# Kernel optimization log

Hardware: AMD Instinct MI355X
Metric: run time of the kernel (lower is better)

## Reference

```python
import jax, jax.numpy as jnp
import numpy as np

D = 2048        # input_size / model dim
H = 2816        # hidden_size per expert (GLU -> w1 has 2*H rows)
E = 8           # num_experts
M = 4096        # tokens (batch*seq)


def setup_inputs() -> dict:
    key = jax.random.key(0)
    k1, k2, k3, k4, k5 = jax.random.split(key, 5)
    x = jax.random.normal(k1, (M, D), dtype=jnp.float32)
    # ParallelExperts init: uniform(-1/fan_in_dim, 1/fan_in_dim); scale kept simple here
    w1 = jax.random.uniform(k2, (E, 2 * H, D), dtype=jnp.float32, minval=-1.0, maxval=1.0) / (2 * H)
    w2 = jax.random.uniform(k3, (E, D, H), dtype=jnp.float32, minval=-1.0, maxval=1.0) / D
    router_w = jax.random.normal(k4, (E, D), dtype=jnp.float32) * (1.0 / np.sqrt(D))
    bias = jnp.zeros((D,), dtype=jnp.float32)
    return {"x": x, "w1": w1, "w2": w2, "router_w": router_w, "bias": bias, "top_k": 2}


def _moe_forward(x, w1, w2, router_w, bias, top_k):
    # Router: logits -> softmax (fp32) -> top-k -> renormalize (fused_moe semantics)
    logits = x @ router_w.T                                # [M, E]
    probs = jax.nn.softmax(logits.astype(jnp.float32), axis=-1)
    topk_w, topk_ids = jax.lax.top_k(probs, top_k)         # [M, k]
    topk_w = topk_w / jnp.sum(topk_w, axis=-1, keepdims=True)
    # Dense combine weights [M, E]: gate weight if expert selected, else 0
    m = x.shape[0]
    combine = jnp.zeros((m, w1.shape[0]), dtype=x.dtype)
    combine = combine.at[jnp.arange(m)[:, None], topk_ids].add(topk_w.astype(x.dtype))
    # Grouped expert GEMMs, expressed as a loop over the small fixed expert set.
    # Contribution of expert e is masked by combine[:, e] (zero for unrouted tokens).
    y = jnp.zeros_like(x)
    hdim = w2.shape[2]
    for e in range(w1.shape[0]):
        g = x @ w1[e].T                                    # [M, 2H]
        h = jax.nn.silu(g[:, :hdim]) * g[:, hdim:]          # silu_and_mul (GLU)
        y = y + combine[:, e:e + 1] * (h @ w2[e].T)         # [M, D]
    return y + bias


def reference(x, w1, w2, router_w, bias, top_k):
    return _moe_forward(x, w1, w2, router_w, bias, top_k)
```

## Files before the change

kernel.cpp:

```cpp
#include <hip/hip_runtime.h>
#include <hip/hip_bf16.h>
#include <stdint.h>

#define M_TOK 4096
#define DDIM  2048
#define HDIM  2816
#define NEXP  8
#define PMAX  10240
#define MAXTILES 40
#define NB1   22
#define NB2   16
#define NKT1  32
#define NKT2  44

typedef __attribute__((ext_vector_type(8))) short short8;
typedef __attribute__((ext_vector_type(4))) float f32x4;

#define GLD16(g, l) __builtin_amdgcn_global_load_lds(                              \
    (const __attribute__((address_space(1))) unsigned int*)(g),                    \
    (__attribute__((address_space(3))) unsigned int*)(l), 16, 0, 0)

#define VMCNT(n) asm volatile("s_waitcnt vmcnt(" #n ")" ::: "memory")

__device__ __forceinline__ unsigned short f2bf(float f) {
  unsigned int u = __float_as_uint(f);
  u += 0x7fffu + ((u >> 16) & 1u);
  return (unsigned short)(u >> 16);
}
__device__ __forceinline__ float bf2f(unsigned short u) {
  return __uint_as_float(((unsigned)u) << 16);
}

#define STGA(TT, PP, S)                                                            \
  { size_t kb_ = (size_t)(TT) * 128 + (S) * 64;                                    \
    char* d_ = ldsp + (PP) * 32768 + (S) * 16384;                                  \
    GLD16(aS0 + kb_, d_ + tid * 16); GLD16(aS1 + kb_, d_ + 8192 + tid * 16); }

#define STGB(TT, PP, S)                                                            \
  { size_t kb_ = (size_t)(TT) * 128 + (S) * 64;                                    \
    char* d_ = ldsp + 65536 + (PP) * 32768 + (S) * 16384;                          \
    GLD16(bS0 + kb_, d_ + tid * 16); GLD16(bS1 + kb_, d_ + 8192 + tid * 16); }

#define DSRA(PP, S, M)                                                             \
  { const char* ab_ = ldsp + (PP) * 32768 + (S) * 16384;                           \
    _Pragma("unroll") for (int j_ = 0; j_ < 4; ++j_)                               \
      av[j_] = *(const short8*)(ab_ + aoff[(M) * 4 + j_]); }

#define DSRB(PP, S)                                                                \
  { const char* bb_ = ldsp + 65536 + (PP) * 32768 + (S) * 16384;                   \
    _Pragma("unroll") for (int j_ = 0; j_ < 4; ++j_)                               \
      bv[j_] = *(const short8*)(bb_ + boff[j_]); }

#define MMA16(M)                                                                   \
  { __builtin_amdgcn_s_setprio(1);                                                 \
    _Pragma("unroll") for (int j_ = 0; j_ < 4; ++j_)                               \
      _Pragma("unroll") for (int n_ = 0; n_ < 4; ++n_)                             \
        acc[(M) * 4 + j_][n_] =                                                    \
          __builtin_amdgcn_mfma_f32_16x16x32_bf16(av[j_], bv[n_], acc[(M)*4+j_][n_], 0, 0, 0); \
    __builtin_amdgcn_s_setprio(0); }

#define KTILE(T, P, S0, S1, S2, S3, VM)                                            \
  { DSRA(P, 0, 0); DSRB(P, 0);                                                     \
    if (S0) STGA((T) + 1, (P) ^ 1, 1);                                             \
    __builtin_amdgcn_s_barrier(); MMA16(0); __builtin_amdgcn_s_barrier();          \
    DSRA(P, 0, 1);                                                                 \
    if (S1) STGB((T) + 2, P, 0);                                                   \
    __builtin_amdgcn_s_barrier(); MMA16(1); __builtin_amdgcn_s_barrier();          \
    DSRA(P, 1, 0); DSRB(P, 1);                                                     \
    if (S2) STGA((T) + 2, P, 0);                                                   \
    __builtin_amdgcn_s_barrier(); MMA16(0); __builtin_amdgcn_s_barrier();          \
    DSRA(P, 1, 1);                                                                 \
    if (S3) STGB((T) + 2, P, 1);                                                   \
    __builtin_amdgcn_s_barrier(); MMA16(1);                                        \
    VMCNT(VM);                                                                     \
    __builtin_amdgcn_s_barrier(); }

__global__ void init_k(int* __restrict__ tok, int* __restrict__ counts, int* __restrict__ cursors) {
  int i = blockIdx.x * blockDim.x + threadIdx.x;
  if (i < PMAX) tok[i] = -1;
  if (i < NEXP) { counts[i] = 0; cursors[i] = 0; }
}

__global__ __launch_bounds__(256) void router_cvt_k(const float4* __restrict__ x4,
                                                    const float4* __restrict__ rw4,
                                                    ushort4* __restrict__ xb4,
                                                    float* __restrict__ wgt,
                                                    int* __restrict__ eid,
                                                    int* __restrict__ counts,
                                                    const float4* __restrict__ w14,
                                                    ushort4* __restrict__ w1b4,
                                                    const float4* __restrict__ w24,
                                                    ushort4* __restrict__ w2b4) {
  int lane = threadIdx.x & 63;
  int wv = threadIdx.x >> 6;
  int t = blockIdx.x * 4 + wv;
  int base = t * (DDIM / 4);
  float acc[NEXP];
#pragma unroll
  for (int e = 0; e < NEXP; ++e) acc[e] = 0.f;
#pragma unroll
  for (int j = 0; j < DDIM / 4 / 64; ++j) {
    float4 v = x4[base + j * 64 + lane];
    ushort4 o;
    o.x = f2bf(v.x); o.y = f2bf(v.y); o.z = f2bf(v.z); o.w = f2bf(v.w);
    xb4[base + j * 64 + lane] = o;
#pragma unroll
    for (int e = 0; e < NEXP; ++e) {
      float4 w = rw4[e * (DDIM / 4) + j * 64 + lane];
      acc[e] += v.x * w.x + v.y * w.y + v.z * w.z + v.w * w.w;
    }
  }
#pragma unroll
  for (int e = 0; e < NEXP; ++e) {
#pragma unroll
    for (int s = 32; s > 0; s >>= 1) acc[e] += __shfl_xor(acc[e], s, 64);
  }
  if (lane == 0) {
    float mx = acc[0];
#pragma unroll
    for (int e = 1; e < NEXP; ++e) mx = fmaxf(mx, acc[e]);
    float p[NEXP];
#pragma unroll
    for (int e = 0; e < NEXP; ++e) p[e] = expf(acc[e] - mx);
    int e0 = 0; float p0 = p[0];
#pragma unroll
    for (int e = 1; e < NEXP; ++e) if (p[e] > p0) { p0 = p[e]; e0 = e; }
    int e1 = -1; float p1 = -1.f;
#pragma unroll
    for (int e = 0; e < NEXP; ++e) if (e != e0 && p[e] > p1) { p1 = p[e]; e1 = e; }
    float s = p0 + p1;
    wgt[2 * t] = p0 / s; wgt[2 * t + 1] = p1 / s;
    eid[2 * t] = e0;     eid[2 * t + 1] = e1;
    atomicAdd(&counts[e0], 1);
    atomicAdd(&counts[e1], 1);
  }
  const int n1 = NEXP * 2 * HDIM * DDIM / 4;
  const int n2 = NEXP * DDIM * HDIM / 4;
  const int stride = (M_TOK / 4) * 256;
  int id = blockIdx.x * 256 + threadIdx.x;
  for (int i = id; i < n1; i += stride) {
    float4 v = w14[i];
    ushort4 o;
    o.x = f2bf(v.x); o.y = f2bf(v.y); o.z = f2bf(v.z); o.w = f2bf(v.w);
    w1b4[i] = o;
  }
  for (int i = id; i < n2; i += stride) {
    float4 v = w24[i];
    ushort4 o;
    o.x = f2bf(v.x); o.y = f2bf(v.y); o.z = f2bf(v.z); o.w = f2bf(v.w);
    w2b4[i] = o;
  }
}

__global__ void offsets_k(const int* __restrict__ counts, int* __restrict__ offs,
                          int* __restrict__ tile2exp, int* __restrict__ tilerow,
                          int* __restrict__ ntiles) {
  if (threadIdx.x == 0 && blockIdx.x == 0) {
    int o = 0, nt = 0;
    for (int e = 0; e < NEXP; ++e) {
      offs[e] = o;
      int c = counts[e];
      int pt = (c + 255) >> 8;
      for (int i = 0; i < pt; ++i) { tile2exp[nt] = e; tilerow[nt] = o + i * 256; ++nt; }
      o += pt << 8;
    }
    offs[NEXP] = o;
    ntiles[0] = nt;
  }
}

__global__ void scatter_k(const int* __restrict__ eid, const int* __restrict__ offs,
                          int* __restrict__ cursors, int* __restrict__ tok,
                          int* __restrict__ slot) {
  int t = blockIdx.x * blockDim.x + threadIdx.x;
  if (t >= M_TOK) return;
#pragma unroll
  for (int k = 0; k < 2; ++k) {
    int e = eid[2 * t + k];
    int p = offs[e] + atomicAdd(&cursors[e], 1);
    tok[p] = t;
    slot[2 * t + k] = p;
  }
}

__global__ __launch_bounds__(512, 1) void gemm1_k(const unsigned short* __restrict__ xb,
                                                  const unsigned short* __restrict__ w1b,
                                                  const int* __restrict__ tok,
                                                  const int* __restrict__ tile2exp,
                                                  const int* __restrict__ tilerow,
                                                  const int* __restrict__ ntiles,
                                                  unsigned short* __restrict__ h) {
  __shared__ char ldsp[131072];
  int mt = blockIdx.x;
  if (mt >= ntiles[0]) return;
  int e = tile2exp[mt], r0 = tilerow[mt];
  int n0 = blockIdx.y * 128;
  int tid = threadIdx.x, lane = tid & 63;
  int wv = tid >> 6, wm = wv >> 2, wn = wv & 3;
  int l15 = lane & 15, g = lane >> 4;

  int row0 = tid >> 2, g0 = (tid & 3) ^ ((row0 >> 1) & 3);
  int row1 = row0 + 128;
  int t0 = tok[r0 + row0]; if (t0 < 0) t0 = 0;
  int t1 = tok[r0 + row1]; if (t1 < 0) t1 = 0;
  const char* aS0 = (const char*)xb + (size_t)t0 * (DDIM * 2) + g0 * 16;
  const char* aS1 = (const char*)xb + (size_t)t1 * (DDIM * 2) + g0 * 16;
  size_t w1r0 = (size_t)e * (2 * HDIM) + (size_t)(n0 + row0);
  size_t w1r1 = (size_t)e * (2 * HDIM) + (size_t)(HDIM + n0 + row0);
  const char* bS0 = (const char*)w1b + w1r0 * (DDIM * 2) + g0 * 16;
  const char* bS1 = (const char*)w1b + w1r1 * (DDIM * 2) + g0 * 16;

  int aoff[8], boff[4];
#pragma unroll
  for (int mi = 0; mi < 8; ++mi) {
    int r = wm * 128 + mi * 16 + l15;
    aoff[mi] = r * 64 + ((g ^ ((r >> 1) & 3)) << 4);
  }
#pragma unroll
  for (int ni = 0; ni < 4; ++ni) {
    int r = wn * 64 + ni * 16 + l15;
    boff[ni] = r * 64 + ((g ^ ((r >> 1) & 3)) << 4);
  }

  f32x4 acc[8][4];
#pragma unroll
  for (int mi = 0; mi < 8; ++mi)
#pragma unroll
    for (int ni = 0; ni < 4; ++ni) acc[mi][ni] = (f32x4)(0.f);

  short8 av[4], bv[4];

  STGA(0, 0, 0); STGB(0, 0, 0); STGA(0, 0, 1); STGB(0, 0, 1);
  STGB(1, 1, 0); STGA(1, 1, 0); STGB(1, 1, 1);
  VMCNT(6);
  __builtin_amdgcn_s_barrier();

#pragma unroll 1
  for (int t = 0; t < NKT1 - 2; t += 2) {
    KTILE(t, 0, 1, 1, 1, 1, 6);
    KTILE(t + 1, 1, 1, 1, 1, 1, 6);
  }
  KTILE(NKT1 - 2, 0, 1, 0, 0, 0, 0);
  KTILE(NKT1 - 1, 1, 0, 0, 0, 0, 0);

  __syncthreads();
  float* xch = (float*)ldsp;
  int rbase = (lane >> 4) * 4;
  if (wn >= 2) {
    int uc0 = (wn - 2) * 64;
#pragma unroll
    for (int mi = 0; mi < 8; ++mi)
#pragma unroll
      for (int ni = 0; ni < 4; ++ni)
#pragma unroll
        for (int j = 0; j < 4; ++j) {
          int r = wm * 128 + mi * 16 + rbase + j;
          int c = uc0 + ni * 16 + l15;
          int cs = c ^ ((r & 3) << 2) ^ ((r & 1) << 4);
          xch[r * 128 + cs] = acc[mi][ni][j];
        }
  }
  __syncthreads();
  if (wn < 2) {
#pragma unroll
    for (int mi = 0; mi < 8; ++mi)
#pragma unroll
      for (int ni = 0; ni < 4; ++ni)
#pragma unroll
        for (int j = 0; j < 4; ++j) {
          int r = wm * 128 + mi * 16 + rbase + j;
          int c = wn * 64 + ni * 16 + l15;
          int cs = c ^ ((r & 3) << 2) ^ ((r & 1) << 4);
          float gg = acc[mi][ni][j];
          float u = xch[r * 128 + cs];
          float sv = gg / (1.f + expf(-gg));
          h[(size_t)(r0 + r) * HDIM + n0 + c] = f2bf(sv * u);
        }
  }
}

__global__ __launch_bounds__(256, 2) void gemm2_k(const unsigned short* __restrict__ h,
                                                  const unsigned short* __restrict__ w2b,
                                                  const int* __restrict__ tile2exp,
                                                  const int* __restrict__ tilerow,
                                                  const int* __restrict__ ntiles,
                                                  unsigned short* __restrict__ yp) {
  __shared__ char ldsp[49152];
  int mt = blockIdx.x;
  if (mt >= ntiles[0]) return;
  int e = tile2exp[mt], r0 = tilerow[mt];
  int n0 = blockIdx.y * 128;
  int tid = threadIdx.x, lane = tid & 63;
  int wv = tid >> 6, wm = wv >> 1, wn = wv & 1;
  int l15 = lane & 15, lq = lane >> 4;

  int sg = tid & 7, srow = tid >> 3;
  unsigned int aOff[8], bOff[4];
#pragma unroll
  for (int j = 0; j < 8; ++j) {
    int r = j * 32 + srow;
    aOff[j] = (unsigned int)(r0 + r) * (HDIM * 2) + (unsigned int)((sg ^ (r & 7)) << 4);
  }
#pragma unroll
  for (int j = 0; j < 4; ++j) {
    int r = j * 32 + srow;
    bOff[j] = (unsigned int)(e * DDIM + n0 + r) * (HDIM * 2) + (unsigned int)((sg ^ (r & 7)) << 4);
  }

  int aRd[8], bRd[4];
#pragma unroll
  for (int i = 0; i < 8; ++i) {
    int r = wm * 128 + i * 16 + l15;
    aRd[i] = r * 128 + ((lq ^ (r & 7)) << 4);
  }
#pragma unroll
  for (int i = 0; i < 4; ++i) {
    int r = wn * 64 + i * 16 + l15;
    bRd[i] = r * 128 + ((lq ^ (r & 7)) << 4);
  }

  f32x4 acc[8][4];
#pragma unroll
  for (int mi = 0; mi < 8; ++mi)
#pragma unroll
    for (int ni = 0; ni < 4; ++ni) acc[mi][ni] = (f32x4)(0.f);

  const char* hB = (const char*)h;
  const char* wB = (const char*)w2b;

#pragma unroll 1
  for (int kt = 0; kt < NKT2; ++kt) {
    __syncthreads();
    unsigned int kb = (unsigned int)kt * 128;
#pragma unroll
    for (int j = 0; j < 8; ++j) GLD16(hB + aOff[j] + kb, ldsp + j * 4096 + tid * 16);
#pragma unroll
    for (int j = 0; j < 4; ++j) GLD16(wB + bOff[j] + kb, ldsp + 32768 + j * 4096 + tid * 16);
    VMCNT(0);
    __syncthreads();
#pragma unroll
    for (int kh = 0; kh < 2; ++kh) {
      int kx = kh << 6;
      short8 a[8], b[4];
#pragma unroll
      for (int i = 0; i < 8; ++i) a[i] = *(const short8*)(ldsp + (aRd[i] ^ kx));
#pragma unroll
      for (int i = 0; i < 4; ++i) b[i] = *(const short8*)(ldsp + 32768 + (bRd[i] ^ kx));
      __builtin_amdgcn_s_setprio(1);
#pragma unroll
      for (int mi = 0; mi < 8; ++mi)
#pragma unroll
        for (int ni = 0; ni < 4; ++ni)
          acc[mi][ni] = __builtin_amdgcn_mfma_f32_16x16x32_bf16(a[mi], b[ni], acc[mi][ni], 0, 0, 0);
      __builtin_amdgcn_s_setprio(0);
    }
  }

#pragma unroll
  for (int mi = 0; mi < 8; ++mi)
#pragma unroll
    for (int ni = 0; ni < 4; ++ni)
#pragma unroll
      for (int j = 0; j < 4; ++j) {
        int r = r0 + wm * 128 + mi * 16 + lq * 4 + j;
        int c = n0 + wn * 64 + ni * 16 + l15;
        yp[(size_t)r * DDIM + c] = f2bf(acc[mi][ni][j]);
      }
}

__global__ void combine_k(const unsigned short* __restrict__ yp, const float* __restrict__ wgt,
                          const int* __restrict__ slot, const float* __restrict__ bias,
                          float* __restrict__ out) {
  int idx = blockIdx.x * blockDim.x + threadIdx.x;
  int t = idx >> 8, q = (idx & 255) * 8;
  float w0 = wgt[2 * t], w1 = wgt[2 * t + 1];
  int s0 = slot[2 * t], s1 = slot[2 * t + 1];
  short8 a8 = *(const short8*)(yp + (size_t)s0 * DDIM + q);
  short8 b8 = *(const short8*)(yp + (size_t)s1 * DDIM + q);
  float* op = out + (size_t)t * DDIM + q;
#pragma unroll
  for (int k = 0; k < 8; ++k) {
    float av = bf2f((unsigned short)a8[k]);
    float bv = bf2f((unsigned short)b8[k]);
    op[k] = w0 * av + w1 * bv + bias[q + k];
  }
}

extern "C" void kernel_launch(void* const* d_in, const int* in_sizes, int n_in,
                              void* d_out, int out_size, void* d_ws, size_t ws_size,
                              hipStream_t stream) {
  const float* x    = (const float*)d_in[0];
  const float* w1   = (const float*)d_in[1];
  const float* w2   = (const float*)d_in[2];
  const float* rw   = (const float*)d_in[3];
  const float* bias = (const float*)d_in[4];
  float* out = (float*)d_out;

  char* ws = (char*)d_ws;
  size_t off = 0;
  auto alloc = [&](size_t bytes) -> void* {
    void* p = ws + off;
    off = (off + bytes + 255) & ~(size_t)255;
    return p;
  };
  unsigned short* w1b = (unsigned short*)alloc((size_t)NEXP * 2 * HDIM * DDIM * 2);
  unsigned short* w2b = (unsigned short*)alloc((size_t)NEXP * DDIM * HDIM * 2);
  unsigned short* xb  = (unsigned short*)alloc((size_t)M_TOK * DDIM * 2);
  unsigned short* h   = (unsigned short*)alloc((size_t)PMAX * HDIM * 2);
  unsigned short* yp  = (unsigned short*)alloc((size_t)PMAX * DDIM * 2);
  float* wgt          = (float*)alloc((size_t)M_TOK * 2 * 4);
  int* eid            = (int*)alloc((size_t)M_TOK * 2 * 4);
  int* slot           = (int*)alloc((size_t)M_TOK * 2 * 4);
  int* tok            = (int*)alloc((size_t)PMAX * 4);
  int* counts         = (int*)alloc(64 * 4);
  int* cursors        = (int*)alloc(64 * 4);
  int* offs           = (int*)alloc(64 * 4);
  int* ntiles         = (int*)alloc(64 * 4);
  int* tile2exp       = (int*)alloc(128 * 4);
  int* tilerow        = (int*)alloc(128 * 4);

  hipLaunchKernelGGL(init_k, dim3((PMAX + 255) / 256), dim3(256), 0, stream, tok, counts, cursors);
  hipLaunchKernelGGL(router_cvt_k, dim3(M_TOK / 4), dim3(256), 0, stream,
                     (const float4*)x, (const float4*)rw, (ushort4*)xb, wgt, eid, counts,
                     (const float4*)w1, (ushort4*)w1b, (const float4*)w2, (ushort4*)w2b);
  hipLaunchKernelGGL(offsets_k, dim3(1), dim3(64), 0, stream, counts, offs,
                     tile2exp, tilerow, ntiles);
  hipLaunchKernelGGL(scatter_k, dim3((M_TOK + 255) / 256), dim3(256), 0, stream, eid, offs, cursors, tok, slot);
  hipLaunchKernelGGL(gemm1_k, dim3(MAXTILES, NB1), dim3(512), 0, stream,
                     xb, w1b, tok, tile2exp, tilerow, ntiles, h);
  hipLaunchKernelGGL(gemm2_k, dim3(MAXTILES, NB2), dim3(256), 0, stream,
                     h, w2b, tile2exp, tilerow, ntiles, yp);
  hipLaunchKernelGGL(combine_k, dim3(M_TOK * (DDIM / 8) / 256), dim3(256), 0, stream, yp, wgt, slot, bias, out);
}
```

Before: 757.5 us.

## Split weight conversion from router and simplify gemm1 to single-buffered 256-thread tiles

Moves the fp32-to-bf16 weight conversion out of the router kernel into a separate grid-stride kernel that processes two elements per thread. gemm1 is rewritten from a 512-thread, double-buffered, 256x256 tile pipeline to a 256-thread kernel with a 256x128 tile (64 gate and 64 up columns), a single LDS buffer, and two blocks per CU. Each K step loads, waits fully and synchronizes before the MFMAs, so load and compute no longer overlap within a block. The change counts on the extra resident block to hide memory latency instead.

```diff
diff --git a/kernel.cpp b/kernel.cpp
--- a/kernel.cpp
+++ b/kernel.cpp
@@ -8,7 +8,7 @@
 #define NEXP  8
 #define PMAX  10240
 #define MAXTILES 40
-#define NB1   22
+#define NB1   44
 #define NB2   16
 #define NKT1  32
 #define NKT2  44
@@ -31,49 +31,28 @@
   return __uint_as_float(((unsigned)u) << 16);
 }
 
-#define STGA(TT, PP, S)                                                            \
-  { size_t kb_ = (size_t)(TT) * 128 + (S) * 64;                                    \
-    char* d_ = ldsp + (PP) * 32768 + (S) * 16384;                                  \
-    GLD16(aS0 + kb_, d_ + tid * 16); GLD16(aS1 + kb_, d_ + 8192 + tid * 16); }
-
-#define STGB(TT, PP, S)                                                            \
-  { size_t kb_ = (size_t)(TT) * 128 + (S) * 64;                                    \
-    char* d_ = ldsp + 65536 + (PP) * 32768 + (S) * 16384;                          \
-    GLD16(bS0 + kb_, d_ + tid * 16); GLD16(bS1 + kb_, d_ + 8192 + tid * 16); }
-
-#define DSRA(PP, S, M)                                                             \
-  { const char* ab_ = ldsp + (PP) * 32768 + (S) * 16384;                           \
-    _Pragma("unroll") for (int j_ = 0; j_ < 4; ++j_)                               \
-      av[j_] = *(const short8*)(ab_ + aoff[(M) * 4 + j_]); }
-
-#define DSRB(PP, S)                                                                \
-  { const char* bb_ = ldsp + 65536 + (PP) * 32768 + (S) * 16384;                   \
-    _Pragma("unroll") for (int j_ = 0; j_ < 4; ++j_)                               \
-      bv[j_] = *(const short8*)(bb_ + boff[j_]); }
-
-#define MMA16(M)                                                                   \
-  { __builtin_amdgcn_s_setprio(1);                                                 \
-    _Pragma("unroll") for (int j_ = 0; j_ < 4; ++j_)                               \
-      _Pragma("unroll") for (int n_ = 0; n_ < 4; ++n_)                             \
-        acc[(M) * 4 + j_][n_] =                                                    \
-          __builtin_amdgcn_mfma_f32_16x16x32_bf16(av[j_], bv[n_], acc[(M)*4+j_][n_], 0, 0, 0); \
-    __builtin_amdgcn_s_setprio(0); }
-
-#define KTILE(T, P, S0, S1, S2, S3, VM)                                            \
-  { DSRA(P, 0, 0); DSRB(P, 0);                                                     \
-    if (S0) STGA((T) + 1, (P) ^ 1, 1);                                             \
-    __builtin_amdgcn_s_barrier(); MMA16(0); __builtin_amdgcn_s_barrier();          \
-    DSRA(P, 0, 1);                                                                 \
-    if (S1) STGB((T) + 2, P, 0);                                                   \
-    __builtin_amdgcn_s_barrier(); MMA16(1); __builtin_amdgcn_s_barrier();          \
-    DSRA(P, 1, 0); DSRB(P, 1);                                                     \
-    if (S2) STGA((T) + 2, P, 0);                                                   \
-    __builtin_amdgcn_s_barrier(); MMA16(0); __builtin_amdgcn_s_barrier();          \
-    DSRA(P, 1, 1);                                                                 \
-    if (S3) STGB((T) + 2, P, 1);                                                   \
-    __builtin_amdgcn_s_barrier(); MMA16(1);                                        \
-    VMCNT(VM);                                                                     \
-    __builtin_amdgcn_s_barrier(); }
+__global__ void cvt2_bf16_k(const float4* __restrict__ in1, ushort4* __restrict__ out1, int n1,
+                            const float4* __restrict__ in2, ushort4* __restrict__ out2, int n2) {
+  const int stride = gridDim.x * blockDim.x;
+  const int total = n1 + n2;
+  int i = blockIdx.x * blockDim.x + threadIdx.x;
+  for (; i + stride < total; i += 2 * stride) {
+    int ia = i, ib = i + stride;
+    float4 va = (ia < n1) ? in1[ia] : in2[ia - n1];
+    float4 vb = (ib < n1) ? in1[ib] : in2[ib - n1];
+    ushort4 oa, ob;
+    oa.x = f2bf(va.x); oa.y = f2bf(va.y); oa.z = f2bf(va.z); oa.w = f2bf(va.w);
+    ob.x = f2bf(vb.x); ob.y = f2bf(vb.y); ob.z = f2bf(vb.z); ob.w = f2bf(vb.w);
+    if (ia < n1) out1[ia] = oa; else out2[ia - n1] = oa;
+    if (ib < n1) out1[ib] = ob; else out2[ib - n1] = ob;
+  }
+  if (i < total) {
+    float4 v = (i < n1) ? in1[i] : in2[i - n1];
+    ushort4 o;
+    o.x = f2bf(v.x); o.y = f2bf(v.y); o.z = f2bf(v.z); o.w = f2bf(v.w);
+    if (i < n1) out1[i] = o; else out2[i - n1] = o;
+  }
+}
 
 __global__ void init_k(int* __restrict__ tok, int* __restrict__ counts, int* __restrict__ cursors) {
   int i = blockIdx.x * blockDim.x + threadIdx.x;
@@ -81,16 +60,12 @@
   if (i < NEXP) { counts[i] = 0; cursors[i] = 0; }
 }
 
-__global__ __launch_bounds__(256) void router_cvt_k(const float4* __restrict__ x4,
-                                                    const float4* __restrict__ rw4,
-                                                    ushort4* __restrict__ xb4,
-                                                    float* __restrict__ wgt,
-                                                    int* __restrict__ eid,
-                                                    int* __restrict__ counts,
-                                                    const float4* __restrict__ w14,
-                                                    ushort4* __restrict__ w1b4,
-                                                    const float4* __restrict__ w24,
-                                                    ushort4* __restrict__ w2b4) {
+__global__ __launch_bounds__(256) void router_k(const float4* __restrict__ x4,
+                                                const float4* __restrict__ rw4,
+                                                ushort4* __restrict__ xb4,
+                                                float* __restrict__ wgt,
+                                                int* __restrict__ eid,
+                                                int* __restrict__ counts) {
   int lane = threadIdx.x & 63;
   int wv = threadIdx.x >> 6;
   int t = blockIdx.x * 4 + wv;
@@ -133,22 +108,6 @@
     eid[2 * t] = e0;     eid[2 * t + 1] = e1;
     atomicAdd(&counts[e0], 1);
     atomicAdd(&counts[e1], 1);
-  }
-  const int n1 = NEXP * 2 * HDIM * DDIM / 4;
-  const int n2 = NEXP * DDIM * HDIM / 4;
-  const int stride = (M_TOK / 4) * 256;
-  int id = blockIdx.x * 256 + threadIdx.x;
-  for (int i = id; i < n1; i += stride) {
-    float4 v = w14[i];
-    ushort4 o;
-    o.x = f2bf(v.x); o.y = f2bf(v.y); o.z = f2bf(v.z); o.w = f2bf(v.w);
-    w1b4[i] = o;
-  }
-  for (int i = id; i < n2; i += stride) {
-    float4 v = w24[i];
-    ushort4 o;
-    o.x = f2bf(v.x); o.y = f2bf(v.y); o.z = f2bf(v.z); o.w = f2bf(v.w);
-    w2b4[i] = o;
   }
 }
 
@@ -183,43 +142,47 @@
   }
 }
 
-__global__ __launch_bounds__(512, 1) void gemm1_k(const unsigned short* __restrict__ xb,
+__global__ __launch_bounds__(256, 2) void gemm1_k(const unsigned short* __restrict__ xb,
                                                   const unsigned short* __restrict__ w1b,
                                                   const int* __restrict__ tok,
                                                   const int* __restrict__ tile2exp,
                                                   const int* __restrict__ tilerow,
                                                   const int* __restrict__ ntiles,
                                                   unsigned short* __restrict__ h) {
-  __shared__ char ldsp[131072];
+  __shared__ char ldsp[65536];
   int mt = blockIdx.x;
   if (mt >= ntiles[0]) return;
   int e = tile2exp[mt], r0 = tilerow[mt];
-  int n0 = blockIdx.y * 128;
+  int n0 = blockIdx.y * 64;
   int tid = threadIdx.x, lane = tid & 63;
-  int wv = tid >> 6, wm = wv >> 2, wn = wv & 3;
-  int l15 = lane & 15, g = lane >> 4;
-
-  int row0 = tid >> 2, g0 = (tid & 3) ^ ((row0 >> 1) & 3);
-  int row1 = row0 + 128;
-  int t0 = tok[r0 + row0]; if (t0 < 0) t0 = 0;
-  int t1 = tok[r0 + row1]; if (t1 < 0) t1 = 0;
-  const char* aS0 = (const char*)xb + (size_t)t0 * (DDIM * 2) + g0 * 16;
-  const char* aS1 = (const char*)xb + (size_t)t1 * (DDIM * 2) + g0 * 16;
-  size_t w1r0 = (size_t)e * (2 * HDIM) + (size_t)(n0 + row0);
-  size_t w1r1 = (size_t)e * (2 * HDIM) + (size_t)(HDIM + n0 + row0);
-  const char* bS0 = (const char*)w1b + w1r0 * (DDIM * 2) + g0 * 16;
-  const char* bS1 = (const char*)w1b + w1r1 * (DDIM * 2) + g0 * 16;
-
-  int aoff[8], boff[4];
-#pragma unroll
-  for (int mi = 0; mi < 8; ++mi) {
-    int r = wm * 128 + mi * 16 + l15;
-    aoff[mi] = r * 64 + ((g ^ ((r >> 1) & 3)) << 4);
-  }
-#pragma unroll
-  for (int ni = 0; ni < 4; ++ni) {
-    int r = wn * 64 + ni * 16 + l15;
-    boff[ni] = r * 64 + ((g ^ ((r >> 1) & 3)) << 4);
+  int wv = tid >> 6, wm = wv >> 1, wn = wv & 1;
+  int l15 = lane & 15, lq = lane >> 4;
+
+  int sg = tid & 7, srow = tid >> 3;
+  unsigned int aOff[8], bOff[4];
+#pragma unroll
+  for (int j = 0; j < 8; ++j) {
+    int r = j * 32 + srow;
+    int t = tok[r0 + r]; if (t < 0) t = 0;
+    aOff[j] = (unsigned int)t * (DDIM * 2) + (unsigned int)((sg ^ (r & 7)) << 4);
+  }
+#pragma unroll
+  for (int j = 0; j < 4; ++j) {
+    int r = j * 32 + srow;
+    int w1row = e * (2 * HDIM) + (r < 64 ? n0 + r : HDIM + n0 + (r - 64));
+    bOff[j] = (unsigned int)w1row * (DDIM * 2) + (unsigned int)((sg ^ (r & 7)) << 4);
+  }
+
+  int aRd[8], bRd[4];
+#pragma unroll
+  for (int i = 0; i < 8; ++i) {
+    int r = wm * 128 + i * 16 + l15;
+    aRd[i] = r * 128 + ((lq ^ (r & 7)) << 4);
+  }
+#pragma unroll
+  for (int i = 0; i < 4; ++i) {
+    int r = wn * 64 + i * 16 + l15;
+    bRd[i] = r * 128 + ((lq ^ (r & 7)) << 4);
   }
 
   f32x4 acc[8][4];
@@ -228,51 +191,63 @@
 #pragma unroll
     for (int ni = 0; ni < 4; ++ni) acc[mi][ni] = (f32x4)(0.f);
 
-  short8 av[4], bv[4];
-
-  STGA(0, 0, 0); STGB(0, 0, 0); STGA(0, 0, 1); STGB(0, 0, 1);
-  STGB(1, 1, 0); STGA(1, 1, 0); STGB(1, 1, 1);
-  VMCNT(6);
-  __builtin_amdgcn_s_barrier();
+  const char* xB = (const char*)xb;
+  const char* wB = (const char*)w1b;
 
 #pragma unroll 1
-  for (int t = 0; t < NKT1 - 2; t += 2) {
-    KTILE(t, 0, 1, 1, 1, 1, 6);
-    KTILE(t + 1, 1, 1, 1, 1, 1, 6);
-  }
-  KTILE(NKT1 - 2, 0, 1, 0, 0, 0, 0);
-  KTILE(NKT1 - 1, 1, 0, 0, 0, 0, 0);
+  for (int kt = 0; kt < NKT1; ++kt) {
+    __syncthreads();
+    unsigned int kb = (unsigned int)kt * 128;
+#pragma unroll
+    for (int j = 0; j < 8; ++j) GLD16(xB + aOff[j] + kb, ldsp + j * 4096 + tid * 16);
+#pragma unroll
+    for (int j = 0; j < 4; ++j) GLD16(wB + bOff[j] + kb, ldsp + 32768 + j * 4096 + tid * 16);
+    VMCNT(0);
+    __syncthreads();
+#pragma unroll
+    for (int kh = 0; kh < 2; ++kh) {
+      int kx = kh << 6;
+      short8 a[8], b[4];
+#pragma unroll
+      for (int i = 0; i < 8; ++i) a[i] = *(const short8*)(ldsp + (aRd[i] ^ kx));
+#pragma unroll
+      for (int i = 0; i < 4; ++i) b[i] = *(const short8*)(ldsp + 32768 + (bRd[i] ^ kx));
+      __builtin_amdgcn_s_setprio(1);
+#pragma unroll
+      for (int mi = 0; mi < 8; ++mi)
+#pragma unroll
+        for (int ni = 0; ni < 4; ++ni)
+          acc[mi][ni] = __builtin_amdgcn_mfma_f32_16x16x32_bf16(a[mi], b[ni], acc[mi][ni], 0, 0, 0);
+      __builtin_amdgcn_s_setprio(0);
+    }
+  }
 
   __syncthreads();
   float* xch = (float*)ldsp;
-  int rbase = (lane >> 4) * 4;
-  if (wn >= 2) {
-    int uc0 = (wn - 2) * 64;
+  if (wn == 1) {
 #pragma unroll
     for (int mi = 0; mi < 8; ++mi)
 #pragma unroll
       for (int ni = 0; ni < 4; ++ni)
 #pragma unroll
         for (int j = 0; j < 4; ++j) {
-          int r = wm * 128 + mi * 16 + rbase + j;
-          int c = uc0 + ni * 16 + l15;
-          int cs = c ^ ((r & 3) << 2) ^ ((r & 1) << 4);
-          xch[r * 128 + cs] = acc[mi][ni][j];
+          int r = wm * 128 + mi * 16 + lq * 4 + j;
+          int c = ni * 16 + l15;
+          xch[r * 64 + (c ^ (lq << 2))] = acc[mi][ni][j];
         }
   }
   __syncthreads();
-  if (wn < 2) {
+  if (wn == 0) {
 #pragma unroll
     for (int mi = 0; mi < 8; ++mi)
 #pragma unroll
       for (int ni = 0; ni < 4; ++ni)
 #pragma unroll
         for (int j = 0; j < 4; ++j) {
-          int r = wm * 128 + mi * 16 + rbase + j;
-          int c = wn * 64 + ni * 16 + l15;
-          int cs = c ^ ((r & 3) << 2) ^ ((r & 1) << 4);
+          int r = wm * 128 + mi * 16 + lq * 4 + j;
+          int c = ni * 16 + l15;
+          float u = xch[r * 64 + (c ^ (lq << 2))];
           float gg = acc[mi][ni][j];
-          float u = xch[r * 128 + cs];
           float sv = gg / (1.f + expf(-gg));
           h[(size_t)(r0 + r) * HDIM + n0 + c] = f2bf(sv * u);
         }
@@ -420,13 +395,15 @@
   int* tilerow        = (int*)alloc(128 * 4);
 
   hipLaunchKernelGGL(init_k, dim3((PMAX + 255) / 256), dim3(256), 0, stream, tok, counts, cursors);
-  hipLaunchKernelGGL(router_cvt_k, dim3(M_TOK / 4), dim3(256), 0, stream,
-                     (const float4*)x, (const float4*)rw, (ushort4*)xb, wgt, eid, counts,
-                     (const float4*)w1, (ushort4*)w1b, (const float4*)w2, (ushort4*)w2b);
+  hipLaunchKernelGGL(cvt2_bf16_k, dim3(4096), dim3(256), 0, stream,
+                     (const float4*)w1, (ushort4*)w1b, (int)((size_t)NEXP * 2 * HDIM * DDIM / 4),
+                     (const float4*)w2, (ushort4*)w2b, (int)((size_t)NEXP * DDIM * HDIM / 4));
+  hipLaunchKernelGGL(router_k, dim3(M_TOK / 4), dim3(256), 0, stream,
+                     (const float4*)x, (const float4*)rw, (ushort4*)xb, wgt, eid, counts);
   hipLaunchKernelGGL(offsets_k, dim3(1), dim3(64), 0, stream, counts, offs,
                      tile2exp, tilerow, ntiles);
   hipLaunchKernelGGL(scatter_k, dim3((M_TOK + 255) / 256), dim3(256), 0, stream, eid, offs, cursors, tok, slot);
-  hipLaunchKernelGGL(gemm1_k, dim3(MAXTILES, NB1), dim3(512), 0, stream,
+  hipLaunchKernelGGL(gemm1_k, dim3(MAXTILES, NB1), dim3(256), 0, stream,
                      xb, w1b, tok, tile2exp, tilerow, ntiles, h);
   hipLaunchKernelGGL(gemm2_k, dim3(MAXTILES, NB2), dim3(256), 0, stream,
                      h, w2b, tile2exp, tilerow, ntiles, yp);
```

After: 765.4 us. About the same (+1.0%).
